# Kernel tuning notes

Measured on AMD Instinct MI355X. Metric: run time of the kernel, lower is better.

Reference implementation:

```python
import jax, jax.numpy as jnp
import numpy as np

HIDDEN = 768
NUM_HEADS = 8
NUM_CELLS = 16384
MAX_HDRS = 8
NUM_HEADERS = 512
LN_EPS = 1e-5


def setup_inputs() -> dict:
    key = jax.random.key(0)
    ks = jax.random.split(key, 16)
    s = 0.02
    D = HIDDEN
    return {
        "cell_value_embeddings": jax.random.normal(ks[0], (NUM_CELLS, D), jnp.float32),
        "header_embeddings": jax.random.normal(ks[1], (NUM_HEADERS, D), jnp.float32),
        "cell_to_header_map": jax.random.randint(ks[2], (NUM_CELLS, MAX_HDRS), 0, NUM_HEADERS),
        "cell_positions": jax.random.randint(ks[3], (NUM_CELLS, 2), 0, 100),
        # nn.MultiheadAttention params
        "in_proj_w": jax.random.normal(ks[4], (3 * D, D), jnp.float32) * s,
        "in_proj_b": jnp.zeros((3 * D,), jnp.float32),
        "out_w": jax.random.normal(ks[5], (D, D), jnp.float32) * s,
        "out_b": jnp.zeros((D,), jnp.float32),
        # positional embedding tables
        "row_emb": jax.random.normal(ks[6], (100, D), jnp.float32) * s,
        "col_emb": jax.random.normal(ks[7], (100, D), jnp.float32) * s,
        # fusion: Linear(2D->D) + LayerNorm
        "fus_w": jax.random.normal(ks[8], (D, 2 * D), jnp.float32) * s,
        "fus_b": jnp.zeros((D,), jnp.float32),
        "ln_g": jnp.ones((D,), jnp.float32),
        "ln_b": jnp.zeros((D,), jnp.float32),
    }


def _forward(cell_value_embeddings, header_embeddings, in_proj_w, in_proj_b,
             out_w, out_b, row_emb, col_emb, fus_w, fus_b, ln_g, ln_b,
             cell_to_header_map, cell_positions):
    N, D = cell_value_embeddings.shape
    H = cell_to_header_map.shape[1]
    nh, dh = NUM_HEADS, D // NUM_HEADS
    scale = 1.0 / (dh ** 0.5)

    pos = jnp.clip(cell_positions, 0, 99)
    cwp = cell_value_embeddings + row_emb[pos[:, 0]] + col_emb[pos[:, 1]]  # [N,D]

    ids = cell_to_header_map
    mask = ids >= 0                                   # [N,H] valid header slots
    hg = header_embeddings[jnp.where(mask, ids, 0)]   # [N,H,D] gathered K/V inputs

    Wq, Wk, Wv = jnp.split(in_proj_w, 3, axis=0)
    bq, bk, bv = jnp.split(in_proj_b, 3)
    q = (cwp @ Wq.T + bq).reshape(N, nh, dh)          # [N,a,d]
    k = (hg @ Wk.T + bk).reshape(N, H, nh, dh)        # [N,k,a,d]
    v = (hg @ Wv.T + bv).reshape(N, H, nh, dh)

    scores = jnp.einsum('nad,nkad->nak', q, k) * scale          # [N,a,k]
    scores = jnp.where(mask[:, None, :], scores, -1e9)
    attn = jax.nn.softmax(scores, axis=-1)
    attn = jnp.where(mask[:, None, :], attn, 0.0)
    ctx = jnp.einsum('nak,nkad->nad', attn, v).reshape(N, D)
    att_out = ctx @ out_w.T + out_b                    # [N,D]

    comb = jnp.concatenate([cwp, att_out], axis=-1)    # [N,2D]
    h = comb @ fus_w.T + fus_b
    mu = jnp.mean(h, axis=-1, keepdims=True)
    var = jnp.mean((h - mu) ** 2, axis=-1, keepdims=True)
    h = (h - mu) * jax.lax.rsqrt(var + LN_EPS) * ln_g + ln_b
    fused = jax.nn.relu(h)

    has = jnp.any(mask, axis=-1)                       # cells with >=1 valid header
    enriched = jnp.where(has[:, None], fused, cwp)
    weights = jnp.where(mask, attn.mean(axis=1), 0.0)  # head-averaged attn [N,H]
    return enriched, weights


def reference(cell_value_embeddings, header_embeddings, cell_to_header_map,
              cell_positions, in_proj_w, in_proj_b, out_w, out_b, row_emb,
              col_emb, fus_w, fus_b, ln_g, ln_b):
    return _forward(cell_value_embeddings, header_embeddings, in_proj_w,
                    in_proj_b, out_w, out_b, row_emb, col_emb, fus_w, fus_b,
                    ln_g, ln_b, cell_to_header_map, cell_positions)
```

## Files before the change

### kernel.cpp

```cpp
#include <hip/hip_runtime.h>
#include <hip/hip_bf16.h>

#define NCELLS 16384
#define DIM    768
#define NHEADS 8
#define DHEAD  96
#define MAXH   8
#define ND     (NCELLS * DIM)


using bf16 = __hip_bfloat16;
typedef short  short8  __attribute__((ext_vector_type(8)));
typedef short  short4v __attribute__((ext_vector_type(4)));
typedef float  floatx4 __attribute__((ext_vector_type(4)));

__device__ inline short f2b(float f) {
    bf16 h = __float2bfloat16(f);
    unsigned short u; __builtin_memcpy(&u, &h, 2); return (short)u;
}
__device__ inline float b2f(short u) {
    unsigned x = ((unsigned)(unsigned short)u) << 16;
    float f; __builtin_memcpy(&f, &x, 4); return f;
}

__device__ inline short8 ld8(const float* p) {
    floatx4 a = *reinterpret_cast<const floatx4*>(p);
    floatx4 b = *reinterpret_cast<const floatx4*>(p + 4);
    short8 o;
#pragma unroll
    for (int i = 0; i < 4; ++i) { o[i] = f2b(a[i]); o[i + 4] = f2b(b[i]); }
    return o;
}

__device__ __forceinline__ void cp16(const void* g, void* l) {
    __builtin_amdgcn_global_load_lds(
        (const __attribute__((address_space(1))) void*)g,
        (__attribute__((address_space(3))) void*)l, 16, 0, 0);
}

template <int DUAL, int COUT>
__global__ __launch_bounds__(256) void gemm_bf(
    const bf16* __restrict__ A, const bf16* __restrict__ A2,
    const bf16* __restrict__ W, int ldw,
    const float* __restrict__ bias,
    float* __restrict__ Cf, bf16* __restrict__ Cb, int K)
{
    __shared__ short As[128 * 64];
    __shared__ short Bs[128 * 64];
    const int tid = threadIdx.x, wave = tid >> 6, lane = tid & 63;
    const int id = blockIdx.x;
    const int m0 = (id & 127) * 128;
    const int n0 = (id >> 7) * 128;
    const int wr = (wave & 1) * 64, wc = (wave >> 1) * 64;
    const int fr = lane & 15, kg = lane >> 4;

    const int srow = lane >> 3;
    const int scol = (lane & 7) ^ srow;

    floatx4 acc[16];
#pragma unroll
    for (int i = 0; i < 16; ++i) acc[i] = (floatx4){0.f, 0.f, 0.f, 0.f};

    for (int k0 = 0; k0 < K; k0 += 64) {
        const bf16* Ak; int ka;
        if (!DUAL || k0 < DIM) { Ak = A;  ka = k0; }
        else                   { Ak = A2; ka = k0 - DIM; }

        __syncthreads();
#pragma unroll
        for (int i = 0; i < 4; ++i) {
            const int c = i * 4 + wave;
            const int row = c * 8 + srow;
            cp16(Ak + (size_t)(m0 + row) * DIM + ka + scol * 8,
                 &As[c * 512 + lane * 8]);
            cp16(W  + (size_t)(n0 + row) * ldw + k0 + scol * 8,
                 &Bs[c * 512 + lane * 8]);
        }
        __syncthreads();

#pragma unroll
        for (int kk = 0; kk < 2; ++kk) {
            short8 af[4], bfv[4];
#pragma unroll
            for (int i = 0; i < 4; ++i) {
                const int sa = ((kk * 4 + kg) ^ (fr & 7)) * 8;
                af[i]  = *reinterpret_cast<const short8*>(&As[(wr + i * 16 + fr) * 64 + sa]);
                bfv[i] = *reinterpret_cast<const short8*>(&Bs[(wc + i * 16 + fr) * 64 + sa]);
            }
#pragma unroll
            for (int i = 0; i < 4; ++i)
#pragma unroll
                for (int j = 0; j < 4; ++j)
                    acc[i * 4 + j] = __builtin_amdgcn_mfma_f32_16x16x32_bf16(
                        af[i], bfv[j], acc[i * 4 + j], 0, 0, 0);
        }
    }

    const int col_l = lane & 15, row_q = kg * 4;
#pragma unroll
    for (int j = 0; j < 4; ++j) {
        const int col = n0 + wc + j * 16 + col_l;
        const float bv = bias[col];
#pragma unroll
        for (int i = 0; i < 4; ++i) {
#pragma unroll
            for (int r = 0; r < 4; ++r) {
                const int row = m0 + wr + i * 16 + row_q + r;
                const float v = acc[i * 4 + j][r] + bv;
                if (COUT == 0) Cf[(size_t)row * DIM + col] = v;
                else           Cb[(size_t)row * DIM + col] = __float2bfloat16(v);
            }
        }
    }
}

__global__ __launch_bounds__(256) void prep_kernel(
    const float* __restrict__ ce, const int* __restrict__ pos,
    const float* __restrict__ re, const float* __restrict__ co,
    bf16* __restrict__ cwp_b,
    const float* __restrict__ in_proj_w, bf16* __restrict__ Wq_b,
    const float* __restrict__ fus_w,     bf16* __restrict__ Wf_b,
    const float* __restrict__ out_w, const float* __restrict__ out_b,
    const float* __restrict__ fus_b, float* __restrict__ bco,
    const float* __restrict__ hdr, const float* __restrict__ in_proj_b,
    bf16* __restrict__ HKV)
{
    __shared__ short As[64 * 72];
    __shared__ short Bs[64 * 72];
    const int b = blockIdx.x, tid = threadIdx.x;

    if (b < 192) {
        const int m0 = (b & 7) * 64, n0 = (b >> 3) * 64;
        const float* W = in_proj_w + (size_t)DIM * DIM;
        const float* bias = in_proj_b + DIM;
        const int wave = tid >> 6, lane = tid & 63;
        const int lr = tid >> 2, lc = (tid & 3) * 16;
        const int fr = lane & 15, fk = (lane >> 4) * 8;

        floatx4 acc[4];
#pragma unroll
        for (int i = 0; i < 4; ++i) acc[i] = (floatx4){0.f, 0.f, 0.f, 0.f};

        const float* ap = hdr + (size_t)(m0 + lr) * DIM + lc;
        const float* wp = W   + (size_t)(n0 + lr) * DIM + lc;
        short8 a0 = ld8(ap), a1 = ld8(ap + 8);
        short8 w0 = ld8(wp), w1 = ld8(wp + 8);

        for (int it = 0; it < 12; ++it) {
            __syncthreads();
            *reinterpret_cast<short8*>(&As[lr * 72 + lc])     = a0;
            *reinterpret_cast<short8*>(&As[lr * 72 + lc + 8]) = a1;
            *reinterpret_cast<short8*>(&Bs[lr * 72 + lc])     = w0;
            *reinterpret_cast<short8*>(&Bs[lr * 72 + lc + 8]) = w1;
            __syncthreads();
            if (it < 11) {
                const int k0 = (it + 1) * 64;
                a0 = ld8(ap + k0); a1 = ld8(ap + k0 + 8);
                w0 = ld8(wp + k0); w1 = ld8(wp + k0 + 8);
            }
#pragma unroll
            for (int kk = 0; kk < 2; ++kk) {
                short8 af = *reinterpret_cast<const short8*>(
                    &As[(wave * 16 + fr) * 72 + kk * 32 + fk]);
#pragma unroll
                for (int t = 0; t < 4; ++t) {
                    short8 bfv = *reinterpret_cast<const short8*>(
                        &Bs[(t * 16 + fr) * 72 + kk * 32 + fk]);
                    acc[t] = __builtin_amdgcn_mfma_f32_16x16x32_bf16(af, bfv, acc[t], 0, 0, 0);
                }
            }
        }
        const int col_l = lane & 15, row_q = (lane >> 4) * 4;
#pragma unroll
        for (int t = 0; t < 4; ++t) {
            const int col = n0 + t * 16 + col_l;
            const float bv = bias[col];
#pragma unroll
            for (int r = 0; r < 4; ++r) {
                const int row = m0 + wave * 16 + row_q + r;
                HKV[(size_t)row * 1536 + col] = __float2bfloat16(acc[t][r] + bv);
            }
        }
    } else if (b < 336) {
        const int b3 = b - 192;
        const int n0  = (b3 % 12) * 64;
        const int k0t = (b3 / 12) * 64;
        const int wave = tid >> 6, lane = tid & 63;
        const int lr = tid >> 2, lc = (tid & 3) * 16;
        const int fr = lane & 15, fk = (lane >> 4) * 8;

        floatx4 acc[4];
#pragma unroll
        for (int i = 0; i < 4; ++i) acc[i] = (floatx4){0.f, 0.f, 0.f, 0.f};

        const float* ap = fus_w + (size_t)(n0 + lr) * 1536 + 768 + lc;
        const float* bp = out_w + (size_t)lr * DIM + k0t + lc;
        short8 a0 = ld8(ap), a1 = ld8(ap + 8);
        floatx4 q0 = *reinterpret_cast<const floatx4*>(bp);
        floatx4 q1 = *reinterpret_cast<const floatx4*>(bp + 4);
        floatx4 q2 = *reinterpret_cast<const floatx4*>(bp + 8);
        floatx4 q3 = *reinterpret_cast<const floatx4*>(bp + 12);

        for (int it = 0; it < 12; ++it) {
            __syncthreads();
            *reinterpret_cast<short8*>(&As[lr * 72 + lc])     = a0;
            *reinterpret_cast<short8*>(&As[lr * 72 + lc + 8]) = a1;
#pragma unroll
            for (int e = 0; e < 4; ++e) {
                Bs[(lc + e) * 72 + lr]      = f2b(q0[e]);
                Bs[(lc + 4 + e) * 72 + lr]  = f2b(q1[e]);
                Bs[(lc + 8 + e) * 72 + lr]  = f2b(q2[e]);
                Bs[(lc + 12 + e) * 72 + lr] = f2b(q3[e]);
            }
            __syncthreads();
            if (it < 11) {
                const int r0 = (it + 1) * 64;
                a0 = ld8(ap + r0); a1 = ld8(ap + r0 + 8);
                const float* bq = bp + (size_t)r0 * DIM;
                q0 = *reinterpret_cast<const floatx4*>(bq);
                q1 = *reinterpret_cast<const floatx4*>(bq + 4);
                q2 = *reinterpret_cast<const floatx4*>(bq + 8);
                q3 = *reinterpret_cast<const floatx4*>(bq + 12);
            }
#pragma unroll
            for (int kk = 0; kk < 2; ++kk) {
                short8 af = *reinterpret_cast<const short8*>(
                    &As[(wave * 16 + fr) * 72 + kk * 32 + fk]);
#pragma unroll
                for (int t = 0; t < 4; ++t) {
                    short8 bfv = *reinterpret_cast<const short8*>(
                        &Bs[(t * 16 + fr) * 72 + kk * 32 + fk]);
                    acc[t] = __builtin_amdgcn_mfma_f32_16x16x32_bf16(af, bfv, acc[t], 0, 0, 0);
                }
            }
        }
        const int col_l = lane & 15, row_q = (lane >> 4) * 4;
#pragma unroll
        for (int t = 0; t < 4; ++t) {
            const int col = k0t + t * 16 + col_l;
#pragma unroll
            for (int r = 0; r < 4; ++r) {
                const int row = n0 + wave * 16 + row_q + r;
                Wf_b[(size_t)row * 1536 + 768 + col] = __float2bfloat16(acc[t][r]);
            }
        }
    } else if (b < 339) {
        const int n = (b - 336) * 256 + tid;
        const float* wrow = fus_w + (size_t)n * 1536 + 768;
        float acc = fus_b[n];
#pragma unroll 4
        for (int m = 0; m < 768; m += 4) {
            floatx4 wv = *reinterpret_cast<const floatx4*>(wrow + m);
            floatx4 ob = *reinterpret_cast<const floatx4*>(out_b + m);
            acc += wv[0] * ob[0] + wv[1] * ob[1] + wv[2] * ob[2] + wv[3] * ob[3];
        }
        bco[n] = acc;
    } else if (b < 915) {
        const int i = (b - 339) * 256 + tid;
        floatx4 v = *reinterpret_cast<const floatx4*>(in_proj_w + (size_t)i * 4);
        short4v o;
#pragma unroll
        for (int j = 0; j < 4; ++j) o[j] = f2b(v[j]);
        *reinterpret_cast<short4v*>((short*)Wq_b + (size_t)i * 4) = o;
    } else if (b < 1491) {
        const int i  = (b - 915) * 256 + tid;
        const int e0 = i * 4;
        const int n  = e0 / 768;
        const int k  = e0 - n * 768;
        const size_t src = (size_t)n * 1536 + k;
        floatx4 v = *reinterpret_cast<const floatx4*>(fus_w + src);
        short4v o;
#pragma unroll
        for (int j = 0; j < 4; ++j) o[j] = f2b(v[j]);
        *reinterpret_cast<short4v*>((short*)Wf_b + src) = o;
    } else {
        const int gid  = (b - 1491) * 256 + tid;
        const int cell = gid / 96;
        const int off  = (gid % 96) * 8;
        int pr = pos[cell * 2 + 0]; pr = min(max(pr, 0), 99);
        int pc = pos[cell * 2 + 1]; pc = min(max(pc, 0), 99);
        const float* a = ce + (size_t)cell * DIM + off;
        const float* bb = re + (size_t)pr * DIM + off;
        const float* c = co + (size_t)pc * DIM + off;
        floatx4 a0 = *reinterpret_cast<const floatx4*>(a);
        floatx4 a1 = *reinterpret_cast<const floatx4*>(a + 4);
        floatx4 b0 = *reinterpret_cast<const floatx4*>(bb);
        floatx4 b1 = *reinterpret_cast<const floatx4*>(bb + 4);
        floatx4 c0 = *reinterpret_cast<const floatx4*>(c);
        floatx4 c1 = *reinterpret_cast<const floatx4*>(c + 4);
        short8 o;
#pragma unroll
        for (int i = 0; i < 4; ++i) {
            o[i]     = f2b(a0[i] + b0[i] + c0[i]);
            o[i + 4] = f2b(a1[i] + b1[i] + c1[i]);
        }
        *reinterpret_cast<short8*>((short*)cwp_b + (size_t)cell * DIM + off) = o;
    }
}

__global__ __launch_bounds__(256) void attn_w_kernel(
    const bf16* __restrict__ q, bf16* __restrict__ ctx,
    const bf16* __restrict__ HKV, const int* __restrict__ map,
    float* __restrict__ wout)
{
    const int wave = threadIdx.x >> 6, lane = threadIdx.x & 63;
    const int cell = blockIdx.x * 4 + wave;
    const int a = lane >> 3, j = lane & 7;

    int id = map[(size_t)cell * MAXH + j];
    const float msk = (id >= 0) ? 1.f : 0.f;
    id = (id >= 0) ? id : 0;

    const short* kp = (const short*)HKV + (size_t)id * 1536 + a * DHEAD;
    const short* qp = (const short*)q + (size_t)cell * DIM + a * DHEAD;
    float s = 0.f;
#pragma unroll
    for (int c = 0; c < 12; ++c) {
        short8 kv = *reinterpret_cast<const short8*>(kp + c * 8);
        short8 qv = *reinterpret_cast<const short8*>(qp + c * 8);
#pragma unroll
        for (int e = 0; e < 8; ++e) s += b2f(qv[e]) * b2f(kv[e]);
    }
    s *= 0.10206207261596577f;
    s = (msk != 0.f) ? s : -1e9f;

    float m = s;
    m = fmaxf(m, __shfl_xor(m, 1));
    m = fmaxf(m, __shfl_xor(m, 2));
    m = fmaxf(m, __shfl_xor(m, 4));
    float e = expf(s - m) * msk;
    float sum = e;
    sum += __shfl_xor(sum, 1);
    sum += __shfl_xor(sum, 2);
    sum += __shfl_xor(sum, 4);
    const float at = (sum > 0.f) ? e / sum : 0.f;

    float wsum = at;
    wsum += __shfl_xor(wsum, 8);
    wsum += __shfl_xor(wsum, 16);
    wsum += __shfl_xor(wsum, 32);
    if (lane < 8) wout[(size_t)cell * MAXH + lane] = wsum * 0.125f;

    int vid[8];
#pragma unroll
    for (int jj = 0; jj < 8; ++jj) vid[jj] = __shfl(id, jj);

    {
        const int d0 = lane * 8;
        const int ha = lane / 12;
        float acc[8];
#pragma unroll
        for (int e2 = 0; e2 < 8; ++e2) acc[e2] = 0.f;
#pragma unroll
        for (int jj = 0; jj < 8; ++jj) {
            const float w = __shfl(at, ha * 8 + jj);
            short8 vv = *reinterpret_cast<const short8*>(
                (const short*)HKV + (size_t)vid[jj] * 1536 + DIM + d0);
#pragma unroll
            for (int e2 = 0; e2 < 8; ++e2) acc[e2] += w * b2f(vv[e2]);
        }
        short8 o;
#pragma unroll
        for (int e2 = 0; e2 < 8; ++e2) o[e2] = f2b(acc[e2]);
        *reinterpret_cast<short8*>((short*)ctx + (size_t)cell * DIM + d0) = o;
    }

    {
        const int d0 = 512 + (lane & 31) * 8;
        const int ha = d0 / 96;
        float acc[8];
#pragma unroll
        for (int e2 = 0; e2 < 8; ++e2) acc[e2] = 0.f;
#pragma unroll
        for (int jj = 0; jj < 8; ++jj) {
            const float w = __shfl(at, ha * 8 + jj);
            short8 vv = *reinterpret_cast<const short8*>(
                (const short*)HKV + (size_t)vid[jj] * 1536 + DIM + d0);
#pragma unroll
            for (int e2 = 0; e2 < 8; ++e2) acc[e2] += w * b2f(vv[e2]);
        }
        if (lane < 32) {
            short8 o;
#pragma unroll
            for (int e2 = 0; e2 < 8; ++e2) o[e2] = f2b(acc[e2]);
            *reinterpret_cast<short8*>((short*)ctx + (size_t)cell * DIM + d0) = o;
        }
    }
}

__global__ __launch_bounds__(384) void ln_v_kernel(
    float* io, const int* __restrict__ map,
    const float* __restrict__ ce, const int* __restrict__ pos,
    const float* __restrict__ re, const float* __restrict__ co,
    const float* __restrict__ g, const float* __restrict__ b)
{
    const int h = threadIdx.x / 192;
    const int t = threadIdx.x % 192;
    const int cell = blockIdx.x * 2 + h;
    const int wave = t >> 6, lane = t & 63;
    __shared__ float ws_[2][3], wq_[2][3];
    __shared__ int hasf[2];
    if (threadIdx.x < 2) hasf[threadIdx.x] = 0;

    float* hp = io + (size_t)cell * DIM;
    floatx4 v = *reinterpret_cast<const floatx4*>(hp + t * 4);
    float s  = v[0] + v[1] + v[2] + v[3];
    float q2 = v[0]*v[0] + v[1]*v[1] + v[2]*v[2] + v[3]*v[3];
#pragma unroll
    for (int off = 32; off > 0; off >>= 1) {
        s  += __shfl_down(s, off);
        q2 += __shfl_down(q2, off);
    }
    __syncthreads();
    if (t < MAXH && map[cell * MAXH + t] >= 0) hasf[h] = 1;
    if (lane == 0) { ws_[h][wave] = s; wq_[h][wave] = q2; }
    __syncthreads();

    const float mu  = (ws_[h][0] + ws_[h][1] + ws_[h][2]) * (1.f / 768.f);
    const float var = (wq_[h][0] + wq_[h][1] + wq_[h][2]) * (1.f / 768.f) - mu * mu;
    const float inv = rsqrtf(var + 1e-5f);

    if (hasf[h]) {
        floatx4 gv = *reinterpret_cast<const floatx4*>(g + t * 4);
        floatx4 bv = *reinterpret_cast<const floatx4*>(b + t * 4);
        floatx4 o;
#pragma unroll
        for (int e = 0; e < 4; ++e)
            o[e] = fmaxf((v[e] - mu) * inv * gv[e] + bv[e], 0.f);
        *reinterpret_cast<floatx4*>(hp + t * 4) = o;
    } else {
        int pr = pos[cell * 2 + 0]; pr = min(max(pr, 0), 99);
        int pc = pos[cell * 2 + 1]; pc = min(max(pc, 0), 99);
        floatx4 a0 = *reinterpret_cast<const floatx4*>(ce + (size_t)cell * DIM + t * 4);
        floatx4 b0 = *reinterpret_cast<const floatx4*>(re + (size_t)pr * DIM + t * 4);
        floatx4 c0 = *reinterpret_cast<const floatx4*>(co + (size_t)pc * DIM + t * 4);
        floatx4 o;
#pragma unroll
        for (int e = 0; e < 4; ++e) o[e] = a0[e] + b0[e] + c0[e];
        *reinterpret_cast<floatx4*>(hp + t * 4) = o;
    }
}

extern "C" void kernel_launch(void* const* d_in, const int* in_sizes, int n_in,
                              void* d_out, int out_size, void* d_ws, size_t ws_size,
                              hipStream_t stream) {
    (void)in_sizes; (void)n_in; (void)out_size; (void)ws_size;

    const float* cell_emb  = (const float*)d_in[0];
    const float* hdr_emb   = (const float*)d_in[1];
    const int*   map       = (const int*)d_in[2];
    const int*   pos       = (const int*)d_in[3];
    const float* in_proj_w = (const float*)d_in[4];
    const float* in_proj_b = (const float*)d_in[5];
    const float* out_w     = (const float*)d_in[6];
    const float* out_b     = (const float*)d_in[7];
    const float* row_emb   = (const float*)d_in[8];
    const float* col_emb   = (const float*)d_in[9];
    const float* fus_w     = (const float*)d_in[10];
    const float* fus_b     = (const float*)d_in[11];
    const float* ln_g      = (const float*)d_in[12];
    const float* ln_b      = (const float*)d_in[13];
    float* out = (float*)d_out;

    char* ws = (char*)d_ws;
    bf16*  HKV   = (bf16*)ws;
    bf16*  ctx_b = (bf16*)(ws + 1572864);
    bf16*  cwp_b = (bf16*)(ws + 26738688);
    bf16*  Wq_b  = (bf16*)(ws + 51904512);
    float* bco   = (float*)(ws + 53084160);
    bf16*  Wf_b  = (bf16*)(ws + 54263808);
    bf16* q_b = (bf16*)d_out;

    prep_kernel<<<7635, 256, 0, stream>>>(
        cell_emb, pos, row_emb, col_emb, cwp_b,
        in_proj_w, Wq_b, fus_w, Wf_b,
        out_w, out_b, fus_b, bco,
        hdr_emb, in_proj_b, HKV);

    gemm_bf<0, 1><<<768, 256, 0, stream>>>(
        cwp_b, nullptr, Wq_b, DIM, in_proj_b, nullptr, q_b, DIM);

    attn_w_kernel<<<NCELLS / 4, 256, 0, stream>>>(q_b, ctx_b, HKV, map, out + ND);

    gemm_bf<1, 0><<<768, 256, 0, stream>>>(
        cwp_b, ctx_b, Wf_b, 1536, bco, out, nullptr, 1536);

    ln_v_kernel<<<NCELLS / 2, 384, 0, stream>>>(out, map, cell_emb, pos,
                                                row_emb, col_emb, ln_g, ln_b);
}
```

Before: 314.9 us.

## Restructure attention kernel to use two waves per cell with LDS softmax exchange

The attention kernel now gives each cell 128 threads instead of one wave. It issues all K, Q and V loads up front so memory latency overlaps with compute, and passes softmax weights through shared memory instead of shuffles. The V-weighted sum is split across 96 threads, which removes the old second pass where half the lanes sat idle, and the dot-product accumulation is split into four independent chains. The cost is two block barriers, more registers holding preloaded vectors, and a second wave per cell that is partly idle.

```diff
diff --git a/kernel.cpp b/kernel.cpp
--- a/kernel.cpp
+++ b/kernel.cpp
@@ -298,93 +298,95 @@
     }
 }
 
-__global__ __launch_bounds__(256) void attn_w_kernel(
+__global__ __launch_bounds__(256) void attn_s_kernel(
     const bf16* __restrict__ q, bf16* __restrict__ ctx,
     const bf16* __restrict__ HKV, const int* __restrict__ map,
     float* __restrict__ wout)
 {
-    const int wave = threadIdx.x >> 6, lane = threadIdx.x & 63;
-    const int cell = blockIdx.x * 4 + wave;
-    const int a = lane >> 3, j = lane & 7;
-
-    int id = map[(size_t)cell * MAXH + j];
-    const float msk = (id >= 0) ? 1.f : 0.f;
-    id = (id >= 0) ? id : 0;
-
-    const short* kp = (const short*)HKV + (size_t)id * 1536 + a * DHEAD;
-    const short* qp = (const short*)q + (size_t)cell * DIM + a * DHEAD;
-    float s = 0.f;
-#pragma unroll
-    for (int c = 0; c < 12; ++c) {
-        short8 kv = *reinterpret_cast<const short8*>(kp + c * 8);
-        short8 qv = *reinterpret_cast<const short8*>(qp + c * 8);
-#pragma unroll
-        for (int e = 0; e < 8; ++e) s += b2f(qv[e]) * b2f(kv[e]);
-    }
-    s *= 0.10206207261596577f;
-    s = (msk != 0.f) ? s : -1e9f;
-
-    float m = s;
-    m = fmaxf(m, __shfl_xor(m, 1));
-    m = fmaxf(m, __shfl_xor(m, 2));
-    m = fmaxf(m, __shfl_xor(m, 4));
-    float e = expf(s - m) * msk;
-    float sum = e;
-    sum += __shfl_xor(sum, 1);
-    sum += __shfl_xor(sum, 2);
-    sum += __shfl_xor(sum, 4);
-    const float at = (sum > 0.f) ? e / sum : 0.f;
-
-    float wsum = at;
-    wsum += __shfl_xor(wsum, 8);
-    wsum += __shfl_xor(wsum, 16);
-    wsum += __shfl_xor(wsum, 32);
-    if (lane < 8) wout[(size_t)cell * MAXH + lane] = wsum * 0.125f;
-
-    int vid[8];
-#pragma unroll
-    for (int jj = 0; jj < 8; ++jj) vid[jj] = __shfl(id, jj);
-
-    {
-        const int d0 = lane * 8;
-        const int ha = lane / 12;
+    const int h = threadIdx.x >> 7;
+    const int t = threadIdx.x & 127;
+    const int cell = blockIdx.x * 2 + h;
+    __shared__ int   ids[2][MAXH];
+    __shared__ float msk[2][MAXH];
+    __shared__ float at_l[2][64];
+
+    if (t < MAXH) {
+        int id = map[(size_t)cell * MAXH + t];
+        msk[h][t] = (id >= 0) ? 1.f : 0.f;
+        ids[h][t] = (id >= 0) ? id : 0;
+    }
+    __syncthreads();
+
+    short8 kv[12], qv[12], vv[8];
+    const int a = t >> 3, j = t & 7;
+    if (t < 64) {
+        const short* kp = (const short*)HKV + (size_t)ids[h][j] * 1536 + a * DHEAD;
+        const short* qp = (const short*)q + (size_t)cell * DIM + a * DHEAD;
+#pragma unroll
+        for (int c = 0; c < 12; ++c)
+            kv[c] = *reinterpret_cast<const short8*>(kp + c * 8);
+#pragma unroll
+        for (int c = 0; c < 12; ++c)
+            qv[c] = *reinterpret_cast<const short8*>(qp + c * 8);
+    }
+    if (t < 96) {
+        const int d0 = t * 8;
+#pragma unroll
+        for (int jj = 0; jj < 8; ++jj)
+            vv[jj] = *reinterpret_cast<const short8*>(
+                (const short*)HKV + (size_t)ids[h][jj] * 1536 + DIM + d0);
+    }
+
+    if (t < 64) {
+        float s0 = 0.f, s1 = 0.f, s2 = 0.f, s3 = 0.f;
+#pragma unroll
+        for (int c = 0; c < 12; c += 4) {
+#pragma unroll
+            for (int e = 0; e < 8; ++e) {
+                s0 += b2f(qv[c    ][e]) * b2f(kv[c    ][e]);
+                s1 += b2f(qv[c + 1][e]) * b2f(kv[c + 1][e]);
+                s2 += b2f(qv[c + 2][e]) * b2f(kv[c + 2][e]);
+                s3 += b2f(qv[c + 3][e]) * b2f(kv[c + 3][e]);
+            }
+        }
+        float s = ((s0 + s1) + (s2 + s3)) * 0.10206207261596577f;
+        const float mk = msk[h][j];
+        s = (mk != 0.f) ? s : -1e9f;
+        float m = s;
+        m = fmaxf(m, __shfl_xor(m, 1));
+        m = fmaxf(m, __shfl_xor(m, 2));
+        m = fmaxf(m, __shfl_xor(m, 4));
+        float e = expf(s - m) * mk;
+        float sum = e;
+        sum += __shfl_xor(sum, 1);
+        sum += __shfl_xor(sum, 2);
+        sum += __shfl_xor(sum, 4);
+        at_l[h][t] = (sum > 0.f) ? e / sum : 0.f;
+    }
+    __syncthreads();
+
+    if (t < 96) {
+        const int d0 = t * 8, ha = t / 12;
+        float w[8];
+#pragma unroll
+        for (int jj = 0; jj < 8; ++jj) w[jj] = at_l[h][ha * 8 + jj];
         float acc[8];
 #pragma unroll
-        for (int e2 = 0; e2 < 8; ++e2) acc[e2] = 0.f;
-#pragma unroll
-        for (int jj = 0; jj < 8; ++jj) {
-            const float w = __shfl(at, ha * 8 + jj);
-            short8 vv = *reinterpret_cast<const short8*>(
-                (const short*)HKV + (size_t)vid[jj] * 1536 + DIM + d0);
-#pragma unroll
-            for (int e2 = 0; e2 < 8; ++e2) acc[e2] += w * b2f(vv[e2]);
-        }
+        for (int e = 0; e < 8; ++e) acc[e] = 0.f;
+#pragma unroll
+        for (int jj = 0; jj < 8; ++jj)
+#pragma unroll
+            for (int e = 0; e < 8; ++e) acc[e] += w[jj] * b2f(vv[jj][e]);
         short8 o;
 #pragma unroll
-        for (int e2 = 0; e2 < 8; ++e2) o[e2] = f2b(acc[e2]);
+        for (int e = 0; e < 8; ++e) o[e] = f2b(acc[e]);
         *reinterpret_cast<short8*>((short*)ctx + (size_t)cell * DIM + d0) = o;
-    }
-
-    {
-        const int d0 = 512 + (lane & 31) * 8;
-        const int ha = d0 / 96;
-        float acc[8];
-#pragma unroll
-        for (int e2 = 0; e2 < 8; ++e2) acc[e2] = 0.f;
-#pragma unroll
-        for (int jj = 0; jj < 8; ++jj) {
-            const float w = __shfl(at, ha * 8 + jj);
-            short8 vv = *reinterpret_cast<const short8*>(
-                (const short*)HKV + (size_t)vid[jj] * 1536 + DIM + d0);
-#pragma unroll
-            for (int e2 = 0; e2 < 8; ++e2) acc[e2] += w * b2f(vv[e2]);
-        }
-        if (lane < 32) {
-            short8 o;
-#pragma unroll
-            for (int e2 = 0; e2 < 8; ++e2) o[e2] = f2b(acc[e2]);
-            *reinterpret_cast<short8*>((short*)ctx + (size_t)cell * DIM + d0) = o;
-        }
+    } else if (t < 96 + MAXH) {
+        const int jj = t - 96;
+        float s = 0.f;
+#pragma unroll
+        for (int a2 = 0; a2 < NHEADS; ++a2) s += at_l[h][a2 * 8 + jj];
+        wout[(size_t)cell * MAXH + jj] = s * 0.125f;
     }
 }
 
@@ -480,7 +482,7 @@
     gemm_bf<0, 1><<<768, 256, 0, stream>>>(
         cwp_b, nullptr, Wq_b, DIM, in_proj_b, nullptr, q_b, DIM);
 
-    attn_w_kernel<<<NCELLS / 4, 256, 0, stream>>>(q_b, ctx_b, HKV, map, out + ND);
+    attn_s_kernel<<<NCELLS / 2, 256, 0, stream>>>(q_b, ctx_b, HKV, map, out + ND);
 
     gemm_bf<1, 0><<<768, 256, 0, stream>>>(
         cwp_b, ctx_b, Wf_b, 1536, bco, out, nullptr, 1536);
```

Result: faster. 295.0 us (-6.3%).
